# Kernel optimization log

Measured on AMD Instinct MI355X. Metric: run time of the kernel, lower is better.

The kernel has to match this reference:

```python
import jax, jax.numpy as jnp
import numpy as np

DIM = 768
NUM_HEADS = 12
HEAD_DIM = DIM // NUM_HEADS
SCALE = HEAD_DIM ** -0.5
ELEV_SCALE = 1000.0


def setup_inputs() -> dict:
    key = jax.random.key(0)
    ks = jax.random.split(key, 6)
    B, N = 2, 2048
    x = jax.random.normal(ks[0], (B, N, DIM), dtype=jnp.float32)
    # elevation in meters, roughly 0..3000 m
    elevation_patches = jax.random.uniform(ks[1], (B, N), dtype=jnp.float32) * 3000.0
    # torch nn.Linear weights are [out, in]; y = x @ W.T + b
    w_qkv = jax.random.normal(ks[2], (3 * DIM, DIM), dtype=jnp.float32) * (DIM ** -0.5)
    w_proj = jax.random.normal(ks[3], (DIM, DIM), dtype=jnp.float32) * (DIM ** -0.5)
    b_proj = jax.random.normal(ks[4], (DIM,), dtype=jnp.float32) * 0.02
    alpha = jnp.ones((1,), dtype=jnp.float32)
    return {"x": x, "elevation_patches": elevation_patches,
            "w_qkv": w_qkv, "w_proj": w_proj, "b_proj": b_proj, "alpha": alpha}


def _elevation_bias(elev, alpha):
    # elev: [B, N] -> bias [B, N, N]; penalize uphill (elev_j > elev_i)
    diff = (elev[:, None, :] - elev[:, :, None]) / ELEV_SCALE  # [B, N, N]
    bias = -alpha[0] * jax.nn.relu(diff)
    return jnp.clip(bias, -10.0, 0.0)


def reference(x, elevation_patches, w_qkv, w_proj, b_proj, alpha):
    B, N, D = x.shape
    H, Hd = NUM_HEADS, HEAD_DIM
    qkv = x @ w_qkv.T                                   # [B, N, 3D]
    qkv = qkv.reshape(B, N, 3, H, Hd)
    q = jnp.transpose(qkv[:, :, 0], (0, 2, 1, 3))       # [B, H, N, Hd]
    k = jnp.transpose(qkv[:, :, 1], (0, 2, 1, 3))
    v = jnp.transpose(qkv[:, :, 2], (0, 2, 1, 3))
    scores = jnp.einsum('bhnd,bhmd->bhnm', q, k) * SCALE  # [B, H, N, N]
    bias = _elevation_bias(elevation_patches, alpha)       # [B, N, N]
    scores = scores + bias[:, None, :, :]
    attn = jax.nn.softmax(scores, axis=-1)
    out = jnp.einsum('bhnm,bhmd->bhnd', attn, v)           # [B, H, N, Hd]
    out = jnp.transpose(out, (0, 2, 1, 3)).reshape(B, N, D)
    return out @ w_proj.T + b_proj
```

## Files before the change

kernel.cpp:

```cpp
#include <hip/hip_runtime.h>


typedef __attribute__((ext_vector_type(8))) short bf16x8;
typedef __attribute__((ext_vector_type(4))) float f32x4;
typedef __attribute__((ext_vector_type(16))) float f32x16;

__device__ __forceinline__ unsigned short f2bf(float f) {
  unsigned int u = __builtin_bit_cast(unsigned int, f);
  u += 0x7fffu + ((u >> 16) & 1u);
  return (unsigned short)(u >> 16);
}

__device__ __forceinline__ unsigned cvtpk(float lo, float hi) {
  unsigned r;
  asm("v_cvt_pk_bf16_f32 %0, %1, %2" : "=v"(r) : "v"(lo), "v"(hi));
  return r;
}

__device__ __forceinline__ float exp2v(float x) {
  float r;
  asm("v_exp_f32 %0, %1" : "=v"(r) : "v"(x));
  return r;
}

__device__ __forceinline__ int sw8(int row) {
  return ((row ^ (row >> 3)) & 7) << 3;
}

__device__ __forceinline__ void gload16(const unsigned short* g, unsigned short* l) {
  __builtin_amdgcn_global_load_lds(
      (const __attribute__((address_space(1))) unsigned int*)g,
      (__attribute__((address_space(3))) unsigned int*)l, 16, 0, 0);
}

__global__ __launch_bounds__(256)
void cvt2_kernel(const float* __restrict__ a, unsigned short* __restrict__ ao, int na8,
                 const float* __restrict__ b, unsigned short* __restrict__ bo, int nb8) {
  int i = blockIdx.x * 256 + threadIdx.x;
  const float* src; unsigned short* dst;
  if (i < na8) { src = a; dst = ao; }
  else {
    i -= na8;
    if (i >= nb8) return;
    src = b; dst = bo;
  }
  const float4 f0 = ((const float4*)src)[i * 2];
  const float4 f1 = ((const float4*)src)[i * 2 + 1];
  uint4 v;
  v.x = cvtpk(f0.x, f0.y);
  v.y = cvtpk(f0.z, f0.w);
  v.z = cvtpk(f1.x, f1.y);
  v.w = cvtpk(f1.z, f1.w);
  ((uint4*)dst)[i] = v;
}

__global__ __launch_bounds__(256)
void gemm_a32_kernel(const float* __restrict__ Ap,
                     const unsigned short* __restrict__ Bp,
                     unsigned short* __restrict__ Cp, int M, int N, int K) {
  __shared__ __align__(16) unsigned short lds_a[2][128 * 32];
  __shared__ __align__(16) unsigned short lds_b[2][128 * 32];
  const int t = threadIdx.x;
  const int l = t & 63;
  const int w = t >> 6;
  const int wr = w >> 1, wc = w & 1;
  const int bid = blockIdx.x + gridDim.x * blockIdx.y;
  const int xcd = bid & 7;
  const int idx = bid >> 3;
  const int brow = (xcd * 4 + (idx & 3)) * 128;
  const int bcol = (idx >> 2) * 128;
  const int l15 = l & 15, l4 = l >> 4;

  const int srow = t >> 2;
  const int scol = (t & 3) * 8;
  const float* ga = Ap + (size_t)(brow + srow) * K + scol;
  const unsigned short* gb = Bp + (size_t)(bcol + srow) * K + scol;

  f32x4 acc[4][4] = {};
  const int nk = K >> 5;

  float4 fa[4];
  {
    fa[0] = *(const float4*)ga;
    fa[1] = *(const float4*)(ga + 4);
    fa[2] = *(const float4*)(ga + (size_t)64 * K);
    fa[3] = *(const float4*)(ga + (size_t)64 * K + 4);
    unsigned short* lb = lds_b[0] + w * 512;
    gload16(gb, lb);
    gload16(gb + (size_t)64 * K, lb + 2048);
    uint4 u0, u1;
    u0.x = cvtpk(fa[0].x, fa[0].y); u0.y = cvtpk(fa[0].z, fa[0].w);
    u0.z = cvtpk(fa[1].x, fa[1].y); u0.w = cvtpk(fa[1].z, fa[1].w);
    u1.x = cvtpk(fa[2].x, fa[2].y); u1.y = cvtpk(fa[2].z, fa[2].w);
    u1.z = cvtpk(fa[3].x, fa[3].y); u1.w = cvtpk(fa[3].z, fa[3].w);
    *(uint4*)&lds_a[0][srow * 32 + scol] = u0;
    *(uint4*)&lds_a[0][(srow + 64) * 32 + scol] = u1;
  }
  __syncthreads();

  int buf = 0;
  for (int kt = 0; kt < nk; ++kt) {
    const bool more = kt + 1 < nk;
    if (more) {
      const size_t ko = (size_t)(kt + 1) * 32;
      fa[0] = *(const float4*)(ga + ko);
      fa[1] = *(const float4*)(ga + ko + 4);
      fa[2] = *(const float4*)(ga + ko + (size_t)64 * K);
      fa[3] = *(const float4*)(ga + ko + (size_t)64 * K + 4);
      unsigned short* lb = lds_b[buf ^ 1] + w * 512;
      gload16(gb + ko, lb);
      gload16(gb + ko + (size_t)64 * K, lb + 2048);
    }
    bf16x8 af[4], bfr[4];
#pragma unroll
    for (int i = 0; i < 4; ++i) {
      af[i]  = *(const bf16x8*)&lds_a[buf][(wr * 64 + i * 16 + l15) * 32 + l4 * 8];
      bfr[i] = *(const bf16x8*)&lds_b[buf][(wc * 64 + i * 16 + l15) * 32 + l4 * 8];
    }
#pragma unroll
    for (int i = 0; i < 4; ++i)
#pragma unroll
      for (int j = 0; j < 4; ++j)
        acc[i][j] = __builtin_amdgcn_mfma_f32_16x16x32_bf16(af[i], bfr[j], acc[i][j], 0, 0, 0);
    if (more) {
      uint4 u0, u1;
      u0.x = cvtpk(fa[0].x, fa[0].y); u0.y = cvtpk(fa[0].z, fa[0].w);
      u0.z = cvtpk(fa[1].x, fa[1].y); u0.w = cvtpk(fa[1].z, fa[1].w);
      u1.x = cvtpk(fa[2].x, fa[2].y); u1.y = cvtpk(fa[2].z, fa[2].w);
      u1.z = cvtpk(fa[3].x, fa[3].y); u1.w = cvtpk(fa[3].z, fa[3].w);
      *(uint4*)&lds_a[buf ^ 1][srow * 32 + scol] = u0;
      *(uint4*)&lds_a[buf ^ 1][(srow + 64) * 32 + scol] = u1;
    }
    __syncthreads();
    buf ^= 1;
  }

#pragma unroll
  for (int i = 0; i < 4; ++i)
#pragma unroll
    for (int j = 0; j < 4; ++j)
#pragma unroll
      for (int r = 0; r < 4; ++r) {
        const int row = brow + wr * 64 + i * 16 + l4 * 4 + r;
        const int col = bcol + wc * 64 + j * 16 + l15;
        Cp[(size_t)row * N + col] = f2bf(acc[i][j][r]);
      }
}

__global__ __launch_bounds__(256)
void gemm2_kernel(const unsigned short* __restrict__ Ap,
                  const unsigned short* __restrict__ Bp,
                  const float* __restrict__ bias, float* __restrict__ Cp,
                  int M, int N, int K) {
  __shared__ __align__(16) unsigned short lds_a[2][64 * 32];
  __shared__ __align__(16) unsigned short lds_b[2][128 * 32];
  const int t = threadIdx.x;
  const int l = t & 63;
  const int w = t >> 6;
  const int wr = w >> 1, wc = w & 1;
  const int brow = blockIdx.x * 64;
  const int bcol = blockIdx.y * 128;
  const int l15 = l & 15, l4 = l >> 4;

  const int srow = t >> 2;
  const int scol = (t & 3) * 8;
  const unsigned short* ga = Ap + (size_t)(brow + srow) * K + scol;
  const unsigned short* gb = Bp + (size_t)(bcol + srow) * K + scol;

  f32x4 acc[2][4] = {};
  const int nk = K >> 5;

  {
    gload16(ga, lds_a[0] + w * 512);
    unsigned short* lb = lds_b[0] + w * 512;
    gload16(gb, lb);
    gload16(gb + (size_t)64 * K, lb + 2048);
  }
  __syncthreads();

  int buf = 0;
  for (int kt = 0; kt < nk; ++kt) {
    if (kt + 1 < nk) {
      const size_t ko = (size_t)(kt + 1) * 32;
      gload16(ga + ko, lds_a[buf ^ 1] + w * 512);
      unsigned short* lb = lds_b[buf ^ 1] + w * 512;
      gload16(gb + ko, lb);
      gload16(gb + ko + (size_t)64 * K, lb + 2048);
    }
    bf16x8 af[2], bfr[4];
#pragma unroll
    for (int i = 0; i < 2; ++i)
      af[i] = *(const bf16x8*)&lds_a[buf][(wr * 32 + i * 16 + l15) * 32 + l4 * 8];
#pragma unroll
    for (int j = 0; j < 4; ++j)
      bfr[j] = *(const bf16x8*)&lds_b[buf][(wc * 64 + j * 16 + l15) * 32 + l4 * 8];
#pragma unroll
    for (int i = 0; i < 2; ++i)
#pragma unroll
      for (int j = 0; j < 4; ++j)
        acc[i][j] = __builtin_amdgcn_mfma_f32_16x16x32_bf16(af[i], bfr[j], acc[i][j], 0, 0, 0);
    __syncthreads();
    buf ^= 1;
  }

#pragma unroll
  for (int i = 0; i < 2; ++i)
#pragma unroll
    for (int j = 0; j < 4; ++j)
#pragma unroll
      for (int r = 0; r < 4; ++r) {
        const int row = brow + wr * 32 + i * 16 + l4 * 4 + r;
        const int col = bcol + wc * 64 + j * 16 + l15;
        Cp[(size_t)row * N + col] = acc[i][j][r] + bias[col];
      }
}

__global__ __launch_bounds__(512)
void attn_kernel(const unsigned short* __restrict__ qkv,
                 const float* __restrict__ elev,
                 const float* __restrict__ alpha_p,
                 unsigned short* __restrict__ aout) {
  __shared__ __align__(16) unsigned short lds_k[2][64 * 64];
  __shared__ __align__(16) unsigned short lds_vt[2][64 * 64];
  __shared__ __align__(16) float lds_ej[2][64];

  const int t = threadIdx.x;
  const int l = t & 63;
  const int w = t >> 6;
  const int l31 = l & 31;
  const int h = l >> 5;
  const int b = blockIdx.x / 12, hd = blockIdx.x % 12;
  const int q0 = blockIdx.y * 256 + w * 32;

  const float cE = fmaxf(alpha_p[0], 0.f) * (1.4426950408889634f * 1e-3f);
  const float c1 = 0.18033688011112042f;

  const size_t rs = 2304;
  const unsigned short* qbase = qkv + ((size_t)b * 2048) * rs + hd * 64;
  const unsigned short* kbase = qbase + 768;
  const unsigned short* vbase = qbase + 1536;

  bf16x8 qa[4];
  {
    const unsigned short* qp = qbase + (size_t)(q0 + l31) * rs + h * 8;
#pragma unroll
    for (int ks = 0; ks < 4; ++ks) qa[ks] = *(const bf16x8*)(qp + ks * 16);
  }
  const float eiv = elev[(size_t)b * 2048 + q0 + l31] * cE;

  uint4 onesu; onesu.x = onesu.y = onesu.z = onesu.w = 0x3F803F80u;
  const bf16x8 onesf = __builtin_bit_cast(bf16x8, onesu);

  f32x16 o[2] = {};
  f32x16 ps = {};

  const int sr = t >> 3;
  const int sc = (t & 7) * 8;

  uint4 rk, rv;
  float evn = 0.f;

  rk = *(const uint4*)(kbase + (size_t)sr * rs + sc);
  rv = *(const uint4*)(vbase + (size_t)sr * rs + sc);
  if (t < 64) evn = elev[(size_t)b * 2048 + t];
  *(uint4*)&lds_k[0][sr * 64 + (sc ^ sw8(sr))] = rk;
  {
    union { uint4 u; unsigned short s[8]; } vu; vu.u = rv;
#pragma unroll
    for (int j = 0; j < 8; ++j) {
      const int d = sc + j;
      lds_vt[0][d * 64 + (sr ^ sw8(d))] = vu.s[j];
    }
  }
  if (t < 64) lds_ej[0][t] = evn * cE;
  __syncthreads();

#define ATTN_STEP(IT, CUR, PRE)                                                \
  {                                                                            \
    if (PRE) {                                                                 \
      const int kv1 = ((IT) + 1) * 64;                                         \
      rk = *(const uint4*)(kbase + (size_t)(kv1 + sr) * rs + sc);              \
      rv = *(const uint4*)(vbase + (size_t)(kv1 + sr) * rs + sc);              \
      if (t < 64) evn = elev[(size_t)b * 2048 + kv1 + t];                      \
    }                                                                          \
    f32x16 st[2] = {};                                                         \
    __builtin_amdgcn_s_setprio(1);                                             \
    _Pragma("unroll")                                                          \
    for (int kst = 0; kst < 4; ++kst) {                                        \
      const int col = kst * 16 + h * 8;                                        \
      _Pragma("unroll")                                                        \
      for (int mb = 0; mb < 2; ++mb) {                                         \
        const int row = mb * 32 + l31;                                         \
        bf16x8 kf = *(const bf16x8*)&lds_k[CUR][row * 64 + (col ^ sw8(row))];  \
        st[mb] = __builtin_amdgcn_mfma_f32_32x32x16_bf16(kf, qa[kst], st[mb], 0, 0, 0); \
      }                                                                        \
    }                                                                          \
    __builtin_amdgcn_s_setprio(0);                                             \
    bf16x8 pa[4];                                                              \
    _Pragma("unroll")                                                          \
    for (int mb = 0; mb < 2; ++mb) {                                           \
      float p16[16];                                                           \
      _Pragma("unroll")                                                        \
      for (int rr = 0; rr < 4; ++rr) {                                         \
        const float4 ejq = *(const float4*)&lds_ej[CUR][mb * 32 + rr * 8 + h * 4]; \
        _Pragma("unroll")                                                      \
        for (int jl = 0; jl < 4; ++jl) {                                       \
          const int r = rr * 4 + jl;                                           \
          const float bm = __builtin_amdgcn_fmed3f(ejq[jl] - eiv, 0.f, 14.4269504f); \
          p16[r] = exp2v(__builtin_fmaf(st[mb][r], c1, -bm));                  \
        }                                                                      \
      }                                                                        \
      _Pragma("unroll")                                                        \
      for (int ks2 = 0; ks2 < 2; ++ks2) {                                      \
        unsigned u0 = cvtpk(p16[ks2 * 8 + 0], p16[ks2 * 8 + 1]);               \
        unsigned u1 = cvtpk(p16[ks2 * 8 + 2], p16[ks2 * 8 + 3]);               \
        unsigned v0 = cvtpk(p16[ks2 * 8 + 4], p16[ks2 * 8 + 5]);               \
        unsigned v1 = cvtpk(p16[ks2 * 8 + 6], p16[ks2 * 8 + 7]);               \
        asm volatile("v_permlane32_swap_b32 %0, %1" : "+v"(u0), "+v"(v0));     \
        asm volatile("v_permlane32_swap_b32 %0, %1" : "+v"(u1), "+v"(v1));     \
        uint4 fr; fr.x = u0; fr.y = u1; fr.z = v0; fr.w = v1;                  \
        pa[mb * 2 + ks2] = __builtin_bit_cast(bf16x8, fr);                     \
      }                                                                        \
    }                                                                          \
    __builtin_amdgcn_s_setprio(1);                                             \
    _Pragma("unroll")                                                          \
    for (int ks = 0; ks < 4; ++ks) {                                           \
      const int col = ks * 16 + h * 8;                                         \
      _Pragma("unroll")                                                        \
      for (int nb = 0; nb < 2; ++nb) {                                         \
        const int row = nb * 32 + l31;                                         \
        bf16x8 vf = *(const bf16x8*)&lds_vt[CUR][row * 64 + (col ^ sw8(row))]; \
        o[nb] = __builtin_amdgcn_mfma_f32_32x32x16_bf16(pa[ks], vf, o[nb], 0, 0, 0); \
      }                                                                        \
      ps = __builtin_amdgcn_mfma_f32_32x32x16_bf16(pa[ks], onesf, ps, 0, 0, 0); \
    }                                                                          \
    __builtin_amdgcn_s_setprio(0);                                             \
    if (PRE) {                                                                 \
      *(uint4*)&lds_k[1 - (CUR)][sr * 64 + (sc ^ sw8(sr))] = rk;               \
      union { uint4 u; unsigned short s[8]; } vu; vu.u = rv;                   \
      _Pragma("unroll")                                                        \
      for (int j = 0; j < 8; ++j) {                                            \
        const int d = sc + j;                                                  \
        lds_vt[1 - (CUR)][d * 64 + (sr ^ sw8(d))] = vu.s[j];                   \
      }                                                                        \
      if (t < 64) lds_ej[1 - (CUR)][t] = evn * cE;                             \
    }                                                                          \
    __syncthreads();                                                           \
  }

  for (int s = 0; s < 16; ++s) {
    ATTN_STEP(2 * s, 0, true);
    ATTN_STEP(2 * s + 1, 1, s < 15);
  }
#undef ATTN_STEP

  float inv[16];
#pragma unroll
  for (int r = 0; r < 16; ++r) inv[r] = 1.0f / ps[r];
#pragma unroll
  for (int nb = 0; nb < 2; ++nb) {
    const int col = hd * 64 + nb * 32 + l31;
#pragma unroll
    for (int rr = 0; rr < 4; ++rr)
#pragma unroll
      for (int jl = 0; jl < 4; ++jl) {
        const int r = rr * 4 + jl;
        const int q = q0 + rr * 8 + h * 4 + jl;
        aout[((size_t)b * 2048 + q) * 768 + col] = f2bf(o[nb][r] * inv[r]);
      }
  }
}

extern "C" void kernel_launch(void* const* d_in, const int* in_sizes, int n_in,
                              void* d_out, int out_size, void* d_ws, size_t ws_size,
                              hipStream_t stream) {
  const float* x      = (const float*)d_in[0];
  const float* elev   = (const float*)d_in[1];
  const float* w_qkv  = (const float*)d_in[2];
  const float* w_proj = (const float*)d_in[3];
  const float* b_proj = (const float*)d_in[4];
  const float* alpha  = (const float*)d_in[5];
  float* out = (float*)d_out;

  unsigned short* qkvb   = (unsigned short*)d_ws;
  unsigned short* aob    = qkvb + (size_t)4096 * 2304;
  unsigned short* wqkvb  = aob + (size_t)4096 * 768;
  unsigned short* wprojb = wqkvb + (size_t)2304 * 768;

  cvt2_kernel<<<1152, 256, 0, stream>>>(w_qkv, wqkvb, 2304 * 768 / 8,
                                        w_proj, wprojb, 768 * 768 / 8);

  gemm_a32_kernel<<<dim3(32, 18), 256, 0, stream>>>(
      x, wqkvb, qkvb, 4096, 2304, 768);

  attn_kernel<<<dim3(24, 8), 512, 0, stream>>>(qkvb, elev, alpha, aob);

  gemm2_kernel<<<dim3(64, 6), 256, 0, stream>>>(
      aob, wprojb, b_proj, out, 4096, 768, 768);
}
```

Before: 100.4 us.

## Pre-convert x to bf16 and widen QKV GEMM tile to 128x256

The input x is now converted to bf16 in the shared conversion kernel, alongside the weights. The QKV GEMM can then load both operands with direct global-to-LDS loads instead of loading fp32 into registers and converting in the loop. The GEMM tile grows from 128x128 to 128x256, so each wave keeps 4x8 accumulators and fewer blocks are launched (288 instead of 576). The XCD-aware block remapping is dropped, the bf16 x buffer shares space with the attention output buffer, and the extra conversion pass adds global traffic for x.

```diff
diff --git a/kernel.cpp b/kernel.cpp
--- a/kernel.cpp
+++ b/kernel.cpp
@@ -34,16 +34,15 @@
 }
 
 __global__ __launch_bounds__(256)
-void cvt2_kernel(const float* __restrict__ a, unsigned short* __restrict__ ao, int na8,
-                 const float* __restrict__ b, unsigned short* __restrict__ bo, int nb8) {
+void cvt3_kernel(const float* __restrict__ a, unsigned short* __restrict__ ao, int na8,
+                 const float* __restrict__ b, unsigned short* __restrict__ bo, int nb8,
+                 const float* __restrict__ c, unsigned short* __restrict__ co, int nc8) {
   int i = blockIdx.x * 256 + threadIdx.x;
   const float* src; unsigned short* dst;
   if (i < na8) { src = a; dst = ao; }
-  else {
-    i -= na8;
-    if (i >= nb8) return;
-    src = b; dst = bo;
-  }
+  else if ((i -= na8) < nb8) { src = b; dst = bo; }
+  else if ((i -= nb8) < nc8) { src = c; dst = co; }
+  else return;
   const float4 f0 = ((const float4*)src)[i * 2];
   const float4 f1 = ((const float4*)src)[i * 2 + 1];
   uint4 v;
@@ -55,82 +54,64 @@
 }
 
 __global__ __launch_bounds__(256)
-void gemm_a32_kernel(const float* __restrict__ Ap,
-                     const unsigned short* __restrict__ Bp,
-                     unsigned short* __restrict__ Cp, int M, int N, int K) {
+void gemm1_kernel(const unsigned short* __restrict__ Ap,
+                  const unsigned short* __restrict__ Bp,
+                  unsigned short* __restrict__ Cp, int M, int N, int K) {
   __shared__ __align__(16) unsigned short lds_a[2][128 * 32];
-  __shared__ __align__(16) unsigned short lds_b[2][128 * 32];
+  __shared__ __align__(16) unsigned short lds_b[2][256 * 32];
   const int t = threadIdx.x;
   const int l = t & 63;
   const int w = t >> 6;
-  const int wr = w >> 1, wc = w & 1;
-  const int bid = blockIdx.x + gridDim.x * blockIdx.y;
-  const int xcd = bid & 7;
-  const int idx = bid >> 3;
-  const int brow = (xcd * 4 + (idx & 3)) * 128;
-  const int bcol = (idx >> 2) * 128;
+  const int wr = w & 1, wc = w >> 1;
+  const int brow = blockIdx.x * 128;
+  const int bcol = blockIdx.y * 256;
   const int l15 = l & 15, l4 = l >> 4;
 
   const int srow = t >> 2;
   const int scol = (t & 3) * 8;
-  const float* ga = Ap + (size_t)(brow + srow) * K + scol;
+  const unsigned short* ga = Ap + (size_t)(brow + srow) * K + scol;
   const unsigned short* gb = Bp + (size_t)(bcol + srow) * K + scol;
 
-  f32x4 acc[4][4] = {};
+  f32x4 acc[4][8] = {};
   const int nk = K >> 5;
 
-  float4 fa[4];
   {
-    fa[0] = *(const float4*)ga;
-    fa[1] = *(const float4*)(ga + 4);
-    fa[2] = *(const float4*)(ga + (size_t)64 * K);
-    fa[3] = *(const float4*)(ga + (size_t)64 * K + 4);
+    unsigned short* la = lds_a[0] + w * 512;
     unsigned short* lb = lds_b[0] + w * 512;
+    gload16(ga, la);
+    gload16(ga + (size_t)64 * K, la + 2048);
     gload16(gb, lb);
     gload16(gb + (size_t)64 * K, lb + 2048);
-    uint4 u0, u1;
-    u0.x = cvtpk(fa[0].x, fa[0].y); u0.y = cvtpk(fa[0].z, fa[0].w);
-    u0.z = cvtpk(fa[1].x, fa[1].y); u0.w = cvtpk(fa[1].z, fa[1].w);
-    u1.x = cvtpk(fa[2].x, fa[2].y); u1.y = cvtpk(fa[2].z, fa[2].w);
-    u1.z = cvtpk(fa[3].x, fa[3].y); u1.w = cvtpk(fa[3].z, fa[3].w);
-    *(uint4*)&lds_a[0][srow * 32 + scol] = u0;
-    *(uint4*)&lds_a[0][(srow + 64) * 32 + scol] = u1;
+    gload16(gb + (size_t)128 * K, lb + 4096);
+    gload16(gb + (size_t)192 * K, lb + 6144);
   }
   __syncthreads();
 
   int buf = 0;
   for (int kt = 0; kt < nk; ++kt) {
-    const bool more = kt + 1 < nk;
-    if (more) {
+    if (kt + 1 < nk) {
       const size_t ko = (size_t)(kt + 1) * 32;
-      fa[0] = *(const float4*)(ga + ko);
-      fa[1] = *(const float4*)(ga + ko + 4);
-      fa[2] = *(const float4*)(ga + ko + (size_t)64 * K);
-      fa[3] = *(const float4*)(ga + ko + (size_t)64 * K + 4);
+      unsigned short* la = lds_a[buf ^ 1] + w * 512;
       unsigned short* lb = lds_b[buf ^ 1] + w * 512;
+      gload16(ga + ko, la);
+      gload16(ga + ko + (size_t)64 * K, la + 2048);
       gload16(gb + ko, lb);
       gload16(gb + ko + (size_t)64 * K, lb + 2048);
+      gload16(gb + ko + (size_t)128 * K, lb + 4096);
+      gload16(gb + ko + (size_t)192 * K, lb + 6144);
     }
-    bf16x8 af[4], bfr[4];
-#pragma unroll
-    for (int i = 0; i < 4; ++i) {
-      af[i]  = *(const bf16x8*)&lds_a[buf][(wr * 64 + i * 16 + l15) * 32 + l4 * 8];
-      bfr[i] = *(const bf16x8*)&lds_b[buf][(wc * 64 + i * 16 + l15) * 32 + l4 * 8];
-    }
+    bf16x8 af[4], bfr[8];
 #pragma unroll
     for (int i = 0; i < 4; ++i)
-#pragma unroll
-      for (int j = 0; j < 4; ++j)
+      af[i] = *(const bf16x8*)&lds_a[buf][(wr * 64 + i * 16 + l15) * 32 + l4 * 8];
+#pragma unroll
+    for (int j = 0; j < 8; ++j)
+      bfr[j] = *(const bf16x8*)&lds_b[buf][(wc * 128 + j * 16 + l15) * 32 + l4 * 8];
+#pragma unroll
+    for (int i = 0; i < 4; ++i)
+#pragma unroll
+      for (int j = 0; j < 8; ++j)
         acc[i][j] = __builtin_amdgcn_mfma_f32_16x16x32_bf16(af[i], bfr[j], acc[i][j], 0, 0, 0);
-    if (more) {
-      uint4 u0, u1;
-      u0.x = cvtpk(fa[0].x, fa[0].y); u0.y = cvtpk(fa[0].z, fa[0].w);
-      u0.z = cvtpk(fa[1].x, fa[1].y); u0.w = cvtpk(fa[1].z, fa[1].w);
-      u1.x = cvtpk(fa[2].x, fa[2].y); u1.y = cvtpk(fa[2].z, fa[2].w);
-      u1.z = cvtpk(fa[3].x, fa[3].y); u1.w = cvtpk(fa[3].z, fa[3].w);
-      *(uint4*)&lds_a[buf ^ 1][srow * 32 + scol] = u0;
-      *(uint4*)&lds_a[buf ^ 1][(srow + 64) * 32 + scol] = u1;
-    }
     __syncthreads();
     buf ^= 1;
   }
@@ -138,11 +119,11 @@
 #pragma unroll
   for (int i = 0; i < 4; ++i)
 #pragma unroll
-    for (int j = 0; j < 4; ++j)
+    for (int j = 0; j < 8; ++j)
 #pragma unroll
       for (int r = 0; r < 4; ++r) {
         const int row = brow + wr * 64 + i * 16 + l4 * 4 + r;
-        const int col = bcol + wc * 64 + j * 16 + l15;
+        const int col = bcol + wc * 128 + j * 16 + l15;
         Cp[(size_t)row * N + col] = f2bf(acc[i][j][r]);
       }
 }
@@ -383,15 +364,17 @@
   float* out = (float*)d_out;
 
   unsigned short* qkvb   = (unsigned short*)d_ws;
-  unsigned short* aob    = qkvb + (size_t)4096 * 2304;
-  unsigned short* wqkvb  = aob + (size_t)4096 * 768;
+  unsigned short* xb     = qkvb + (size_t)4096 * 2304;
+  unsigned short* aob    = xb;
+  unsigned short* wqkvb  = xb + (size_t)4096 * 768;
   unsigned short* wprojb = wqkvb + (size_t)2304 * 768;
 
-  cvt2_kernel<<<1152, 256, 0, stream>>>(w_qkv, wqkvb, 2304 * 768 / 8,
+  cvt3_kernel<<<2688, 256, 0, stream>>>(x, xb, 4096 * 768 / 8,
+                                        w_qkv, wqkvb, 2304 * 768 / 8,
                                         w_proj, wprojb, 768 * 768 / 8);
 
-  gemm_a32_kernel<<<dim3(32, 18), 256, 0, stream>>>(
-      x, wqkvb, qkvb, 4096, 2304, 768);
+  gemm1_kernel<<<dim3(32, 9), 256, 0, stream>>>(
+      xb, wqkvb, qkvb, 4096, 2304, 768);
 
   attn_kernel<<<dim3(24, 8), 512, 0, stream>>>(qkvb, elev, alpha, aob);
 
```

New measurement: 129.2 us. 28.7% more time.

## Split attention KV range across two blocks and fuse w_proj conversion into gemm2

Applied to the files above, without the earlier changes.

The attention grid gains a z dimension of 2, so each block handles half of the key/value sequence. Unnormalized partial outputs and row sums go to fp32 scratch, using the output buffer as the second slot, and a new combine kernel sums and normalizes them into bf16. This doubles the attention block count from 192 to 384 so more of the CUs are occupied. Separately, gemm2 now reads fp32 w_proj and converts it to bf16 in registers before the LDS store, which drops that part of the conversion kernel. The cost is an extra kernel launch, extra fp32 traffic for the partials, and slower B loads in gemm2.

```diff
diff --git a/kernel.cpp b/kernel.cpp
--- a/kernel.cpp
+++ b/kernel.cpp
@@ -34,24 +34,17 @@
 }
 
 __global__ __launch_bounds__(256)
-void cvt2_kernel(const float* __restrict__ a, unsigned short* __restrict__ ao, int na8,
-                 const float* __restrict__ b, unsigned short* __restrict__ bo, int nb8) {
-  int i = blockIdx.x * 256 + threadIdx.x;
-  const float* src; unsigned short* dst;
-  if (i < na8) { src = a; dst = ao; }
-  else {
-    i -= na8;
-    if (i >= nb8) return;
-    src = b; dst = bo;
-  }
-  const float4 f0 = ((const float4*)src)[i * 2];
-  const float4 f1 = ((const float4*)src)[i * 2 + 1];
+void cvt_kernel(const float* __restrict__ in, unsigned short* __restrict__ out, int n8) {
+  const int i = blockIdx.x * 256 + threadIdx.x;
+  if (i >= n8) return;
+  const float4 f0 = ((const float4*)in)[i * 2];
+  const float4 f1 = ((const float4*)in)[i * 2 + 1];
   uint4 v;
   v.x = cvtpk(f0.x, f0.y);
   v.y = cvtpk(f0.z, f0.w);
   v.z = cvtpk(f1.x, f1.y);
   v.w = cvtpk(f1.z, f1.w);
-  ((uint4*)dst)[i] = v;
+  ((uint4*)out)[i] = v;
 }
 
 __global__ __launch_bounds__(256)
@@ -149,7 +142,7 @@
 
 __global__ __launch_bounds__(256)
 void gemm2_kernel(const unsigned short* __restrict__ Ap,
-                  const unsigned short* __restrict__ Bp,
+                  const float* __restrict__ Bp,
                   const float* __restrict__ bias, float* __restrict__ Cp,
                   int M, int N, int K) {
   __shared__ __align__(16) unsigned short lds_a[2][64 * 32];
@@ -165,27 +158,38 @@
   const int srow = t >> 2;
   const int scol = (t & 3) * 8;
   const unsigned short* ga = Ap + (size_t)(brow + srow) * K + scol;
-  const unsigned short* gb = Bp + (size_t)(bcol + srow) * K + scol;
+  const float* gbf = Bp + (size_t)(bcol + srow) * K + scol;
 
   f32x4 acc[2][4] = {};
   const int nk = K >> 5;
 
+  float4 fb[4];
   {
     gload16(ga, lds_a[0] + w * 512);
-    unsigned short* lb = lds_b[0] + w * 512;
-    gload16(gb, lb);
-    gload16(gb + (size_t)64 * K, lb + 2048);
+    fb[0] = *(const float4*)gbf;
+    fb[1] = *(const float4*)(gbf + 4);
+    fb[2] = *(const float4*)(gbf + (size_t)64 * K);
+    fb[3] = *(const float4*)(gbf + (size_t)64 * K + 4);
+    uint4 u0, u1;
+    u0.x = cvtpk(fb[0].x, fb[0].y); u0.y = cvtpk(fb[0].z, fb[0].w);
+    u0.z = cvtpk(fb[1].x, fb[1].y); u0.w = cvtpk(fb[1].z, fb[1].w);
+    u1.x = cvtpk(fb[2].x, fb[2].y); u1.y = cvtpk(fb[2].z, fb[2].w);
+    u1.z = cvtpk(fb[3].x, fb[3].y); u1.w = cvtpk(fb[3].z, fb[3].w);
+    *(uint4*)&lds_b[0][srow * 32 + scol] = u0;
+    *(uint4*)&lds_b[0][(srow + 64) * 32 + scol] = u1;
   }
   __syncthreads();
 
   int buf = 0;
   for (int kt = 0; kt < nk; ++kt) {
-    if (kt + 1 < nk) {
+    const bool more = kt + 1 < nk;
+    if (more) {
       const size_t ko = (size_t)(kt + 1) * 32;
       gload16(ga + ko, lds_a[buf ^ 1] + w * 512);
-      unsigned short* lb = lds_b[buf ^ 1] + w * 512;
-      gload16(gb + ko, lb);
-      gload16(gb + ko + (size_t)64 * K, lb + 2048);
+      fb[0] = *(const float4*)(gbf + ko);
+      fb[1] = *(const float4*)(gbf + ko + 4);
+      fb[2] = *(const float4*)(gbf + ko + (size_t)64 * K);
+      fb[3] = *(const float4*)(gbf + ko + (size_t)64 * K + 4);
     }
     bf16x8 af[2], bfr[4];
 #pragma unroll
@@ -199,6 +203,15 @@
 #pragma unroll
       for (int j = 0; j < 4; ++j)
         acc[i][j] = __builtin_amdgcn_mfma_f32_16x16x32_bf16(af[i], bfr[j], acc[i][j], 0, 0, 0);
+    if (more) {
+      uint4 u0, u1;
+      u0.x = cvtpk(fb[0].x, fb[0].y); u0.y = cvtpk(fb[0].z, fb[0].w);
+      u0.z = cvtpk(fb[1].x, fb[1].y); u0.w = cvtpk(fb[1].z, fb[1].w);
+      u1.x = cvtpk(fb[2].x, fb[2].y); u1.y = cvtpk(fb[2].z, fb[2].w);
+      u1.z = cvtpk(fb[3].x, fb[3].y); u1.w = cvtpk(fb[3].z, fb[3].w);
+      *(uint4*)&lds_b[buf ^ 1][srow * 32 + scol] = u0;
+      *(uint4*)&lds_b[buf ^ 1][(srow + 64) * 32 + scol] = u1;
+    }
     __syncthreads();
     buf ^= 1;
   }
@@ -219,7 +232,8 @@
 void attn_kernel(const unsigned short* __restrict__ qkv,
                  const float* __restrict__ elev,
                  const float* __restrict__ alpha_p,
-                 unsigned short* __restrict__ aout) {
+                 float* __restrict__ O0, float* __restrict__ O1,
+                 float* __restrict__ psums) {
   __shared__ __align__(16) unsigned short lds_k[2][64 * 64];
   __shared__ __align__(16) unsigned short lds_vt[2][64 * 64];
   __shared__ __align__(16) float lds_ej[2][64];
@@ -231,6 +245,8 @@
   const int h = l >> 5;
   const int b = blockIdx.x / 12, hd = blockIdx.x % 12;
   const int q0 = blockIdx.y * 256 + w * 32;
+  const int z = blockIdx.z;
+  const int s_lo = z * 16, s_hi = s_lo + 16;
 
   const float cE = fmaxf(alpha_p[0], 0.f) * (1.4426950408889634f * 1e-3f);
   const float c1 = 0.18033688011112042f;
@@ -260,19 +276,20 @@
   uint4 rk, rv;
   float evn = 0.f;
 
-  rk = *(const uint4*)(kbase + (size_t)sr * rs + sc);
-  rv = *(const uint4*)(vbase + (size_t)sr * rs + sc);
-  if (t < 64) evn = elev[(size_t)b * 2048 + t];
-  *(uint4*)&lds_k[0][sr * 64 + (sc ^ sw8(sr))] = rk;
   {
+    const int kv0 = s_lo * 64;
+    rk = *(const uint4*)(kbase + (size_t)(kv0 + sr) * rs + sc);
+    rv = *(const uint4*)(vbase + (size_t)(kv0 + sr) * rs + sc);
+    if (t < 64) evn = elev[(size_t)b * 2048 + kv0 + t];
+    *(uint4*)&lds_k[0][sr * 64 + (sc ^ sw8(sr))] = rk;
     union { uint4 u; unsigned short s[8]; } vu; vu.u = rv;
 #pragma unroll
     for (int j = 0; j < 8; ++j) {
       const int d = sc + j;
       lds_vt[0][d * 64 + (sr ^ sw8(d))] = vu.s[j];
     }
-  }
-  if (t < 64) lds_ej[0][t] = evn * cE;
+    if (t < 64) lds_ej[0][t] = evn * cE;
+  }
   __syncthreads();
 
 #define ATTN_STEP(IT, CUR, PRE)                                                \
@@ -348,15 +365,21 @@
     __syncthreads();                                                           \
   }
 
-  for (int s = 0; s < 16; ++s) {
-    ATTN_STEP(2 * s, 0, true);
-    ATTN_STEP(2 * s + 1, 1, s < 15);
+  for (int s = 0; s < 8; ++s) {
+    ATTN_STEP(s_lo + 2 * s, 0, true);
+    ATTN_STEP(s_lo + 2 * s + 1, 1, s < 7);
   }
 #undef ATTN_STEP
 
-  float inv[16];
-#pragma unroll
-  for (int r = 0; r < 16; ++r) inv[r] = 1.0f / ps[r];
+  const int pbase = z * (24 * 2048) + blockIdx.x * 2048;
+  if (l31 == 0) {
+#pragma unroll
+    for (int r = 0; r < 16; ++r) {
+      const int qr = (r & 3) + 8 * (r >> 2) + 4 * h;
+      psums[pbase + q0 + qr] = ps[r];
+    }
+  }
+  float* OD = z ? O1 : O0;
 #pragma unroll
   for (int nb = 0; nb < 2; ++nb) {
     const int col = hd * 64 + nb * 32 + l31;
@@ -364,11 +387,30 @@
     for (int rr = 0; rr < 4; ++rr)
 #pragma unroll
       for (int jl = 0; jl < 4; ++jl) {
-        const int r = rr * 4 + jl;
         const int q = q0 + rr * 8 + h * 4 + jl;
-        aout[((size_t)b * 2048 + q) * 768 + col] = f2bf(o[nb][r] * inv[r]);
+        OD[((size_t)b * 2048 + q) * 768 + col] = o[nb][rr * 4 + jl];
       }
   }
+}
+
+__global__ __launch_bounds__(192)
+void combine_kernel(const float* __restrict__ O0, const float* __restrict__ O1,
+                    const float* __restrict__ psums, unsigned short* __restrict__ aob) {
+  const int row = blockIdx.x;
+  const int b = row >> 11, q = row & 2047;
+  const int c = threadIdx.x * 4;
+  const int hd = c >> 6;
+  const int pidx = (b * 12 + hd) * 2048 + q;
+  const float inv = 1.0f / (psums[pidx] + psums[24 * 2048 + pidx]);
+  const size_t off = (size_t)row * 768 + c;
+  const float4 a = *(const float4*)&O0[off];
+  const float4 d = *(const float4*)&O1[off];
+  ushort4 r;
+  r.x = f2bf((a.x + d.x) * inv);
+  r.y = f2bf((a.y + d.y) * inv);
+  r.z = f2bf((a.z + d.z) * inv);
+  r.w = f2bf((a.w + d.w) * inv);
+  *(ushort4*)&aob[off] = r;
 }
 
 extern "C" void kernel_launch(void* const* d_in, const int* in_sizes, int n_in,
@@ -382,19 +424,22 @@
   const float* alpha  = (const float*)d_in[5];
   float* out = (float*)d_out;
 
-  unsigned short* qkvb   = (unsigned short*)d_ws;
-  unsigned short* aob    = qkvb + (size_t)4096 * 2304;
-  unsigned short* wqkvb  = aob + (size_t)4096 * 768;
-  unsigned short* wprojb = wqkvb + (size_t)2304 * 768;
-
-  cvt2_kernel<<<1152, 256, 0, stream>>>(w_qkv, wqkvb, 2304 * 768 / 8,
-                                        w_proj, wprojb, 768 * 768 / 8);
+  unsigned short* qkvb  = (unsigned short*)d_ws;
+  unsigned short* aob   = qkvb + (size_t)4096 * 2304;
+  unsigned short* wqkvb = aob + (size_t)4096 * 768;
+  float* P0    = (float*)(wqkvb + (size_t)2304 * 768);
+  float* psums = P0 + (size_t)4096 * 768;
+
+  cvt_kernel<<<864, 256, 0, stream>>>(w_qkv, wqkvb, 2304 * 768 / 8);
 
   gemm_a32_kernel<<<dim3(32, 18), 256, 0, stream>>>(
       x, wqkvb, qkvb, 4096, 2304, 768);
 
-  attn_kernel<<<dim3(24, 8), 512, 0, stream>>>(qkvb, elev, alpha, aob);
+  attn_kernel<<<dim3(24, 8, 2), 512, 0, stream>>>(qkvb, elev, alpha,
+                                                  P0, out, psums);
+
+  combine_kernel<<<4096, 192, 0, stream>>>(P0, out, psums, aob);
 
   gemm2_kernel<<<dim3(64, 6), 256, 0, stream>>>(
-      aob, wprojb, b_proj, out, 4096, 768, 768);
-}
+      aob, w_proj, b_proj, out, 4096, 768, 768);
+}
```

Measured after the change: 115.3 us. 1.15x slower.
